# Optimization experiments

Hardware: AMD Instinct MI355X
Metric: run time of the kernel (lower is better)

## Reference

```python
import jax, jax.numpy as jnp
import numpy as np

# ---- static config ----
G = 4          # num graphs
NG = 512       # nodes per graph
N = G * NG     # total nodes
E = 32768      # num edges
IN_DIM = 128
HID = 32
HEADS = 4
HC = HID * HEADS  # 128
OUT_DIM = 32
N_LAYERS = 2
GRID = 500
Q = 20
NEG_SLOPE = 0.2
QUANTILES = jnp.asarray(np.linspace(0.0, 1.0, Q), jnp.float32)  # [Q]


def setup_inputs() -> dict:
    key = jax.random.key(0)
    ks = jax.random.split(key, 32)
    inp = {}
    inp['x'] = jax.random.normal(ks[0], (N, IN_DIM), jnp.float32)
    inp['edge_index'] = jax.random.randint(ks[1], (2, E), 0, N).astype(jnp.int64)
    inp['batch'] = (jnp.arange(N) // NG).astype(jnp.int64)
    # GATConv params (2 layers, both 128 -> 4 heads x 32, concat)
    for l, (kin,) in enumerate([(IN_DIM,), (HC,)]):
        s = 1.0 / np.sqrt(kin)
        inp[f'W{l}'] = jax.random.normal(ks[2 + 4 * l], (kin, HC), jnp.float32) * s
        inp[f'as{l}'] = jax.random.normal(ks[3 + 4 * l], (HEADS, HID), jnp.float32) * s
        inp[f'ad{l}'] = jax.random.normal(ks[4 + 4 * l], (HEADS, HID), jnp.float32) * s
        inp[f'b{l}'] = jnp.zeros((HC,), jnp.float32)
    for l in range(N_LAYERS + 1):
        inp[f'lpW{l}'] = jax.random.normal(ks[10 + 2 * l], (HC, OUT_DIM), jnp.float32) * (1.0 / np.sqrt(HC))
        inp[f'lpb{l}'] = jnp.zeros((OUT_DIM,), jnp.float32)
    for l in range(N_LAYERS + 1):
        inp[f'kW{l}'] = jax.random.normal(ks[16 + 2 * l], (HC * Q, OUT_DIM), jnp.float32) * (1.0 / np.sqrt(HC * Q))
        inp[f'kb{l}'] = jnp.zeros((OUT_DIM,), jnp.float32)
    inp['pool_w'] = jnp.ones((2,), jnp.float32) / 2.0
    inp['beta'] = jax.random.normal(ks[22], (OUT_DIM,), jnp.float32)
    inp['h0'] = jax.random.normal(ks[23], (1,), jnp.float32)
    return inp


def _gat_layer(x, src, dst, W, a_src, a_dst, bias):
    # PyG GATConv (concat=True, add_self_loops=True, negative_slope=0.2), eval mode
    n = x.shape[0]
    xh = (x @ W).reshape(n, HEADS, HID)              # [N,H,C]
    loop = jnp.arange(n)
    s = jnp.concatenate([src, loop])                 # [E+N]
    d = jnp.concatenate([dst, loop])
    al_s = jnp.einsum('nhc,hc->nh', xh, a_src)       # [N,H]
    al_d = jnp.einsum('nhc,hc->nh', xh, a_dst)
    e = jax.nn.leaky_relu(al_s[s] + al_d[d], NEG_SLOPE)   # [E+N,H]
    e_max = jax.ops.segment_max(e, d, num_segments=n)     # stable softmax per dst
    e = jnp.exp(e - e_max[d])
    denom = jax.ops.segment_sum(e, d, num_segments=n)
    alpha = e / (denom[d] + 1e-16)                   # [E+N,H]
    out = jax.ops.segment_sum(alpha[:, :, None] * xh[s], d, num_segments=n)
    return out.reshape(n, HC) + bias


def _kde_per_graph(xg):
    # xg: [Ng, D] -> [D*Q] soft-quantile features via grid KDE
    n = xg.shape[0]
    mn = xg.min(axis=0) - 1e-6                       # [D]
    mx = xg.max(axis=0) + 1e-6
    grid = jnp.linspace(0.0, 1.0, GRID)[:, None] * (mx - mn) + mn   # [Gp,D]
    std = xg.std(axis=0) + 1e-8 / 3
    h = 1.06 * std * float(n) ** (-0.2)              # [D]
    u = (grid[:, None, :] - xg[None, :, :]) / h      # [Gp,Ng,D]  (dominant tensor)
    kern = jnp.exp(-0.5 * u * u) / (h * np.sqrt(2.0 * np.pi))
    density = kern.mean(axis=1)                      # [Gp,D]
    cdf = jnp.cumsum(density, axis=0)
    cdf = cdf / jnp.clip(cdf[-1:], 1e-8)
    dist = jnp.abs(cdf[:, :, None] - QUANTILES)      # [Gp,D,Q]
    w = jax.nn.sigmoid(-100.0 * dist)
    w = w / (w.sum(axis=0, keepdims=True) + 1e-8)
    qv = (grid[:, :, None] * w).sum(axis=0)          # [D,Q]
    return qv.reshape(-1)


def _readout(cur, lpW, lpb, kW, kb, pool_w):
    xr = cur.reshape(G, NG, -1)
    pooled = jnp.stack([xr.mean(axis=1), xr.max(axis=1)], axis=0)   # [2,G,D]
    wp = (pooled * pool_w[:, None, None]).sum(axis=0)               # [G,D]
    h = wp @ lpW + lpb                                              # [G,out]
    kf = jax.vmap(_kde_per_graph)(xr)                               # [G,D*Q]
    return h, kf @ kW + kb


def reference(x, edge_index, batch, W0, as0, ad0, b0, W1, as1, ad1, b1,
              lpW0, lpb0, lpW1, lpb1, lpW2, lpb2,
              kW0, kb0, kW1, kb1, kW2, kb2, pool_w, beta, h0):
    src, dst = edge_index[0], edge_index[1]
    convs = [(W0, as0, ad0, b0), (W1, as1, ad1, b1)]
    lps = [(lpW0, lpb0), (lpW1, lpb1), (lpW2, lpb2)]
    kps = [(kW0, kb0), (kW1, kb1), (kW2, kb2)]
    cur = x
    h_list, kde_list = [], []
    for i in range(N_LAYERS):
        h, kp = _readout(cur, lps[i][0], lps[i][1], kps[i][0], kps[i][1], pool_w)
        h_list.append(h); kde_list.append(kp)
        cur = _gat_layer(cur, src, dst, *convs[i])
        if i != N_LAYERS - 1:
            cur = jax.nn.relu(cur)
    h, kp = _readout(cur, lps[-1][0], lps[-1][1], kps[-1][0], kps[-1][1], pool_w)
    h_list.append(h); kde_list.append(kp)
    main_out = jnp.stack(h_list).mean(axis=0)        # [G,out]
    kde_out = jnp.stack(kde_list).mean(axis=0)
    risk = (main_out + kde_out) @ beta + h0          # [G]
    return risk
```

## Files before the change

kernel.cpp:

```cpp
#include <hip/hip_runtime.h>
#include <math.h>

#define GNUM 4
#define NG 512
#define NN 2048
#define EE 32768
#define HC 128
#define HEADS 4
#define HID 32
#define GRID_PTS 500
#define QN 20
#define ODIM 32
#define MAXE 160

#define LOG2E 1.44269504088896340736f
#define NEG_HALF_LOG2E -0.72134752044448170368f
#define N_POW_M02 0.2871745887492588f
#define SIG_K 144.269504089f

__device__ __forceinline__ float fexp2(float x){ return __builtin_amdgcn_exp2f(x); }
__device__ __forceinline__ float frcp(float x){ return __builtin_amdgcn_rcpf(x); }

struct SmemKDE {
  __align__(16) float2 xs[NG];
  float4 wred4[8];
  float sc[4];
  float wsum[8], woff[9];
  float redw[QN][8], redg[QN][8];
  float qs[QN];
};
struct SmemXW  { float rows[4][HC]; };
struct SmemGat {
  int   ssrc[4][MAXE];
  float sexp[4][MAXE][HEADS];
  float smax[4][HEADS], sfac[4][HEADS];
};
union Smem { SmemKDE kde; SmemXW xw; SmemGat gat; };

__device__ void kde_phase(Smem& sm, const float* __restrict__ cur, int do_relu, int trans,
        const float* __restrict__ kW, const float* __restrict__ kb, float* __restrict__ kacc,
        const float* __restrict__ lpW, const float* __restrict__ lpb,
        const float* __restrict__ poolw, float* __restrict__ macc){
  int b = blockIdx.x;
  int g = b >> 7, d = b & 127;
  int t = threadIdx.x;
  int lane = t & 63, wave = t >> 6;
  float v = trans ? cur[(size_t)d*NN + g*NG + t]
                  : cur[((size_t)g*NG + t)*HC + d];
  if (do_relu) v = fmaxf(v, 0.f);
  sm.kde.xs[t] = make_float2(v, v*v);
  float mn=v, mx=v, smv=v, sq=v*v;
  #pragma unroll
  for (int m=32; m>0; m>>=1){
    mn = fminf(mn, __shfl_xor(mn, m, 64));
    mx = fmaxf(mx, __shfl_xor(mx, m, 64));
    smv += __shfl_xor(smv, m, 64);
    sq += __shfl_xor(sq, m, 64);
  }
  if (lane==0) sm.kde.wred4[wave] = make_float4(mn,mx,smv,sq);
  __syncthreads();
  if (t==0){
    float4 r = sm.kde.wred4[0];
    #pragma unroll
    for (int i=1;i<8;++i){
      float4 bb = sm.kde.wred4[i];
      r.x = fminf(r.x,bb.x); r.y = fmaxf(r.y,bb.y); r.z += bb.z; r.w += bb.w;
    }
    float mean = r.z * (1.f/NG);
    float var  = fmaxf(r.w*(1.f/NG) - mean*mean, 0.f);
    float sd   = sqrtf(var) + (1e-8f/3.f);
    float h    = 1.06f * sd * N_POW_M02;
    float lo = r.x - 1e-6f, hi = r.y + 1e-6f;
    sm.kde.sc[0] = lo;
    sm.kde.sc[1] = (hi-lo)*(1.f/(GRID_PTS-1));
    sm.kde.sc[2] = NEG_HALF_LOG2E/(h*h);
    sm.kde.sc[3] = poolw[0]*mean + poolw[1]*r.y;
  }
  __syncthreads();
  float lo = sm.kde.sc[0], st = sm.kde.sc[1], kk = sm.kde.sc[2];
  float gv = lo + st*(float)t;
  float acc = 0.f;
  if (t < GRID_PTS){
    float c0 = kk*gv*gv, c1 = -2.f*kk*gv;
    const float4* p4 = (const float4*)sm.kde.xs;
    #pragma unroll 4
    for (int i=0;i<NG/2;++i){
      float4 s2 = p4[i];
      acc += fexp2(fmaf(kk, s2.y, fmaf(c1, s2.x, c0)));
      acc += fexp2(fmaf(kk, s2.w, fmaf(c1, s2.z, c0)));
    }
  }
  float sv = acc;
  #pragma unroll
  for (int off=1; off<64; off<<=1){
    float n = __shfl_up(sv, off, 64);
    if (lane >= off) sv += n;
  }
  if (lane==63) sm.kde.wsum[wave] = sv;
  __syncthreads();
  if (t==0){
    float r2 = 0.f;
    #pragma unroll
    for (int i=0;i<8;++i){ sm.kde.woff[i]=r2; r2+=sm.kde.wsum[i]; }
    sm.kde.woff[8]=r2;
  }
  if (t < QN*8){ ((float*)sm.kde.redw)[t]=0.f; ((float*)sm.kde.redg)[t]=0.f; }
  __syncthreads();
  float invt = 1.f/fmaxf(sm.kde.woff[8], 1e-8f);
  float c = (sv + sm.kde.woff[wave]) * invt;
  float cw0 = __shfl(c, 0, 64), cw1 = __shfl(c, 63, 64);
  int qlo = max(0, (int)ceilf((cw0 - 0.17f)*(float)(QN-1)));
  int qhi = min(QN-1, (int)floorf((cw1 + 0.17f)*(float)(QN-1)));
  for (int q=qlo; q<=qhi; ++q){
    float w = 0.f;
    if (t < GRID_PTS){
      float dist = fabsf(c - (float)q*(1.f/(QN-1)));
      w = frcp(1.f + fexp2(SIG_K*dist));
    }
    float gw = gv*w;
    #pragma unroll
    for (int m=32;m>0;m>>=1){
      w  += __shfl_xor(w,  m, 64);
      gw += __shfl_xor(gw, m, 64);
    }
    if (lane==0){ sm.kde.redw[q][wave]=w; sm.kde.redg[q][wave]=gw; }
  }
  __syncthreads();
  if (t < QN){
    float sw=0.f, sgw=0.f;
    #pragma unroll
    for (int i=0;i<8;++i){ sw+=sm.kde.redw[t][i]; sgw+=sm.kde.redg[t][i]; }
    sm.kde.qs[t] = sgw / (sw + 1e-8f);
  }
  __syncthreads();
  if (t < ODIM){
    int shard = (d >> 5) & 3;
    float a = 0.f;
    const float* kwb = kW + (size_t)d*QN*ODIM + t;
    #pragma unroll
    for (int q=0;q<QN;++q) a += sm.kde.qs[q]*kwb[q*ODIM];
    if (d==0) a += kb[t];
    atomicAdd(&kacc[shard*128 + g*ODIM + t], a);
    float bb = sm.kde.sc[3]*lpW[d*ODIM + t];
    if (d==0) bb += lpb[t];
    atomicAdd(&macc[shard*128 + g*ODIM + t], bb);
  }
  __syncthreads();
}

__device__ float gather_core(Smem& sm, int d, int sub, int tl,
        const int* __restrict__ csr, const int* __restrict__ pos,
        const float* __restrict__ als, const float* __restrict__ ald,
        const float* __restrict__ xh, const float* __restrict__ bias){
  int deg = min(pos[d], MAXE-1);
  int E = deg + 1;
  const int* base = csr + d*MAXE;
  float a0 = ald[d*4+0], a1 = ald[d*4+1], a2 = ald[d*4+2], a3 = ald[d*4+3];
  for (int i=tl; i<E; i+=128){
    int s = (i < deg) ? base[i] : d;
    sm.gat.ssrc[sub][i] = s;
    float e0 = als[s*4+0]+a0, e1 = als[s*4+1]+a1, e2 = als[s*4+2]+a2, e3 = als[s*4+3]+a3;
    e0 = (e0>=0.f)? e0 : 0.2f*e0;
    e1 = (e1>=0.f)? e1 : 0.2f*e1;
    e2 = (e2>=0.f)? e2 : 0.2f*e2;
    e3 = (e3>=0.f)? e3 : 0.2f*e3;
    sm.gat.sexp[sub][i][0]=e0; sm.gat.sexp[sub][i][1]=e1;
    sm.gat.sexp[sub][i][2]=e2; sm.gat.sexp[sub][i][3]=e3;
  }
  __syncthreads();
  if (tl < HEADS){
    float m = -INFINITY;
    for (int i=0;i<E;++i) m = fmaxf(m, sm.gat.sexp[sub][i][tl]);
    sm.gat.smax[sub][tl] = m;
  }
  __syncthreads();
  for (int i=tl; i<E; i+=128){
    #pragma unroll
    for (int h=0;h<HEADS;++h)
      sm.gat.sexp[sub][i][h] = fexp2(LOG2E*(sm.gat.sexp[sub][i][h]-sm.gat.smax[sub][h]));
  }
  __syncthreads();
  if (tl < HEADS){
    float sdn = 0.f;
    for (int i=0;i<E;++i) sdn += sm.gat.sexp[sub][i][tl];
    sm.gat.sfac[sub][tl] = 1.f/(sdn + 1e-16f);
  }
  __syncthreads();
  int h = tl >> 5;
  float fac = sm.gat.sfac[sub][h];
  float acc = bias[tl];
  for (int i=0;i<E;++i)
    acc += sm.gat.sexp[sub][i][h]*fac * xh[(size_t)sm.gat.ssrc[sub][i]*HC + tl];
  __syncthreads();
  return acc;
}

__device__ void xw_emit(Smem& sm, int sub, int j, int n,
        const float* __restrict__ W, const float* __restrict__ as_, const float* __restrict__ ad_,
        float* __restrict__ xh, float* __restrict__ als, float* __restrict__ ald){
  float acc = 0.f;
  #pragma unroll 8
  for (int c2=0;c2<HC;++c2)
    acc += sm.xw.rows[sub][c2]*W[(size_t)c2*HC + j];
  xh[(size_t)n*HC + j] = acc;
  int h = j >> 5, cc = j & 31;
  float ps = acc*as_[h*HID+cc], pd = acc*ad_[h*HID+cc];
  #pragma unroll
  for (int m=16;m>0;m>>=1){
    ps += __shfl_xor(ps, m, 32);
    pd += __shfl_xor(pd, m, 32);
  }
  if (cc==0){ als[n*HEADS+h]=ps; ald[n*HEADS+h]=pd; }
}

__device__ void write_transposed(Smem& sm, int t, int n0, float* __restrict__ curT){
  if (t < HC){
    float4 v = make_float4(sm.xw.rows[0][t], sm.xw.rows[1][t],
                           sm.xw.rows[2][t], sm.xw.rows[3][t]);
    *(float4*)(curT + (size_t)t*NN + n0) = v;
  }
}

__global__ __launch_bounds__(1024) void k_zero(int* __restrict__ pos, float* __restrict__ acc){
  int t = threadIdx.x;
  pos[t] = 0; pos[t+1024] = 0;
  acc[t] = 0.f; acc[t+1024] = 0.f;
  if (t < 1024) acc[t+2048] = 0.f;
}

__global__ __launch_bounds__(512) void k_L0(const float* __restrict__ x,
        const float* __restrict__ kW, const float* __restrict__ kb, float* __restrict__ kacc,
        const float* __restrict__ lpW, const float* __restrict__ lpb,
        const float* __restrict__ poolw, float* __restrict__ macc,
        const float* __restrict__ W, const float* __restrict__ as_, const float* __restrict__ ad_,
        float* __restrict__ xh, float* __restrict__ als, float* __restrict__ ald,
        const int* __restrict__ src, const int* __restrict__ dst,
        int* __restrict__ pos, int* __restrict__ csr){
  __shared__ Smem sm;
  int t = threadIdx.x;
  if (blockIdx.x < 512){
    kde_phase(sm, x, 0, 0, kW, kb, kacc, lpW, lpb, poolw, macc);
  } else {
    int b2 = blockIdx.x - 512;
    if (t < 64){
      int e = b2*64 + t;
      int dd = dst[e];
      int pp = atomicAdd(&pos[dd], 1);
      if (pp < MAXE) csr[dd*MAXE + pp] = src[e];
    }
    int sub = t >> 7, j = t & 127;
    int n = b2*4 + sub;
    sm.xw.rows[sub][j] = x[(size_t)n*HC + j];
    __syncthreads();
    xw_emit(sm, sub, j, n, W, as_, ad_, xh, als, ald);
  }
}

__global__ __launch_bounds__(512) void k_G0(const int* __restrict__ csr, const int* __restrict__ pos,
        const float* __restrict__ als_in, const float* __restrict__ ald_in,
        const float* __restrict__ xh_in, const float* __restrict__ bias,
        float* __restrict__ cur1T,
        const float* __restrict__ W1, const float* __restrict__ as1, const float* __restrict__ ad1,
        float* __restrict__ xh2, float* __restrict__ als2, float* __restrict__ ald2){
  __shared__ Smem sm;
  int t = threadIdx.x;
  int sub = t >> 7, tl = t & 127;
  int d = blockIdx.x*4 + sub;
  float acc = gather_core(sm, d, sub, tl, csr, pos, als_in, ald_in, xh_in, bias);
  sm.xw.rows[sub][tl] = fmaxf(acc, 0.f);
  __syncthreads();
  write_transposed(sm, t, blockIdx.x*4, cur1T);
  xw_emit(sm, sub, tl, d, W1, as1, ad1, xh2, als2, ald2);
}

__global__ __launch_bounds__(512) void k_L1(const float* __restrict__ cur1T,
        const float* __restrict__ kW, const float* __restrict__ kb, float* __restrict__ kacc,
        const float* __restrict__ lpW, const float* __restrict__ lpb,
        const float* __restrict__ poolw, float* __restrict__ macc,
        const int* __restrict__ csr, const int* __restrict__ pos,
        const float* __restrict__ als2, const float* __restrict__ ald2,
        const float* __restrict__ xh2, const float* __restrict__ bias,
        float* __restrict__ cur2T){
  __shared__ Smem sm;
  int t = threadIdx.x;
  if (blockIdx.x < 512){
    kde_phase(sm, cur1T, 0, 1, kW, kb, kacc, lpW, lpb, poolw, macc);
  } else {
    int b2 = blockIdx.x - 512;
    int sub = t >> 7, tl = t & 127;
    int d = b2*4 + sub;
    float acc = gather_core(sm, d, sub, tl, csr, pos, als2, ald2, xh2, bias);
    sm.xw.rows[sub][tl] = acc;
    __syncthreads();
    write_transposed(sm, t, b2*4, cur2T);
  }
}

__global__ __launch_bounds__(512) void k_L2(const float* __restrict__ cur2T,
        const float* __restrict__ kW, const float* __restrict__ kb, float* __restrict__ kacc,
        const float* __restrict__ lpW, const float* __restrict__ lpb,
        const float* __restrict__ poolw, float* __restrict__ macc){
  __shared__ Smem sm;
  kde_phase(sm, cur2T, 0, 1, kW, kb, kacc, lpW, lpb, poolw, macc);
}

__global__ void k_final(const float* __restrict__ maccS, const float* __restrict__ kaccS,
                        const float* __restrict__ beta, const float* __restrict__ h0,
                        float* __restrict__ out){
  int t = threadIdx.x;
  int g = t >> 5, o = t & 31;
  __shared__ float sdm[128];
  float s3 = 0.f;
  #pragma unroll
  for (int l=0;l<3;++l)
    #pragma unroll
    for (int s=0;s<4;++s)
      s3 += maccS[l*512 + s*128 + t] + kaccS[l*512 + s*128 + t];
  sdm[t] = s3 * (1.f/3.f) * beta[o];
  __syncthreads();
  if ((t & 31) == 0){
    float s = 0.f;
    #pragma unroll
    for (int i=0;i<32;++i) s += sdm[g*32+i];
    out[g] = s + h0[0];
  }
}

extern "C" void kernel_launch(void* const* d_in, const int* in_sizes, int n_in,
                              void* d_out, int out_size, void* d_ws, size_t ws_size,
                              hipStream_t stream) {
  (void)in_sizes; (void)n_in; (void)out_size; (void)ws_size;
  const float* x    = (const float*)d_in[0];
  const int*   ei   = (const int*)d_in[1];
  const int*   srcp = ei;
  const int*   dstp = ei + EE;
  const float* W[2]   = {(const float*)d_in[3], (const float*)d_in[7]};
  const float* As[2]  = {(const float*)d_in[4], (const float*)d_in[8]};
  const float* Ad[2]  = {(const float*)d_in[5], (const float*)d_in[9]};
  const float* Bi[2]  = {(const float*)d_in[6], (const float*)d_in[10]};
  const float* lpW[3] = {(const float*)d_in[11], (const float*)d_in[13], (const float*)d_in[15]};
  const float* lpb[3] = {(const float*)d_in[12], (const float*)d_in[14], (const float*)d_in[16]};
  const float* kW[3]  = {(const float*)d_in[17], (const float*)d_in[19], (const float*)d_in[21]};
  const float* kb[3]  = {(const float*)d_in[18], (const float*)d_in[20], (const float*)d_in[22]};
  const float* poolw  = (const float*)d_in[23];
  const float* beta   = (const float*)d_in[24];
  const float* h0     = (const float*)d_in[25];
  float* out = (float*)d_out;

  float* ws = (float*)d_ws;
  float* cur1T = ws;
  float* cur2T = cur1T + 262144;
  float* xh    = cur2T + 262144;
  float* xh2   = xh + 262144;
  float* als   = xh2 + 262144;
  float* ald   = als + 8192;
  float* als2  = ald + 8192;
  float* ald2  = als2 + 8192;
  float* maccS = ald2 + 8192;
  float* kaccS = maccS + 1536;
  int*   pos   = (int*)(kaccS + 1536);
  int*   csr   = pos + 2048;

  k_zero<<<1, 1024, 0, stream>>>(pos, maccS);
  k_L0<<<1024, 512, 0, stream>>>(x, kW[0], kb[0], kaccS, lpW[0], lpb[0], poolw, maccS,
                                 W[0], As[0], Ad[0], xh, als, ald,
                                 srcp, dstp, pos, csr);
  k_G0<<<512, 512, 0, stream>>>(csr, pos, als, ald, xh, Bi[0], cur1T,
                                W[1], As[1], Ad[1], xh2, als2, ald2);
  k_L1<<<1024, 512, 0, stream>>>(cur1T, kW[1], kb[1], kaccS+512, lpW[1], lpb[1], poolw, maccS+512,
                                 csr, pos, als2, ald2, xh2, Bi[1], cur2T);
  k_L2<<<512, 512, 0, stream>>>(cur2T, kW[2], kb[2], kaccS+1024, lpW[2], lpb[2], poolw, maccS+1024);
  k_final<<<1, 128, 0, stream>>>(maccS, kaccS, beta, h0, out);
}
```

Before: 201.1 us.

## Bucket KDE samples and evaluate only those within kernel radius per wave

```diff
diff --git a/kernel.cpp b/kernel.cpp
--- a/kernel.cpp
+++ b/kernel.cpp
@@ -12,6 +12,7 @@
 #define QN 20
 #define ODIM 32
 #define MAXE 160
+#define NBUK 16
 
 #define LOG2E 1.44269504088896340736f
 #define NEG_HALF_LOG2E -0.72134752044448170368f
@@ -24,10 +25,11 @@
 struct SmemKDE {
   __align__(16) float2 xs[NG];
   float4 wred4[8];
-  float sc[4];
+  float sc[8];
   float wsum[8], woff[9];
   float redw[QN][8], redg[QN][8];
   float qs[QN];
+  int bcnt[NBUK], bstart[NBUK+1], bcur[NBUK];
 };
 struct SmemXW  { float rows[4][HC]; };
 struct SmemGat {
@@ -48,7 +50,6 @@
   float v = trans ? cur[(size_t)d*NN + g*NG + t]
                   : cur[((size_t)g*NG + t)*HC + d];
   if (do_relu) v = fmaxf(v, 0.f);
-  sm.kde.xs[t] = make_float2(v, v*v);
   float mn=v, mx=v, smv=v, sq=v*v;
   #pragma unroll
   for (int m=32; m>0; m>>=1){
@@ -58,6 +59,7 @@
     sq += __shfl_xor(sq, m, 64);
   }
   if (lane==0) sm.kde.wred4[wave] = make_float4(mn,mx,smv,sq);
+  if (t < NBUK) sm.kde.bcnt[t] = 0;
   __syncthreads();
   if (t==0){
     float4 r = sm.kde.wred4[0];
@@ -75,19 +77,41 @@
     sm.kde.sc[1] = (hi-lo)*(1.f/(GRID_PTS-1));
     sm.kde.sc[2] = NEG_HALF_LOG2E/(h*h);
     sm.kde.sc[3] = poolw[0]*mean + poolw[1]*r.y;
+    sm.kde.sc[4] = (float)NBUK/(hi-lo);
+    sm.kde.sc[5] = 5.f*h;
   }
   __syncthreads();
   float lo = sm.kde.sc[0], st = sm.kde.sc[1], kk = sm.kde.sc[2];
+  float bscale = sm.kde.sc[4], R = sm.kde.sc[5];
+  int bkt = min(NBUK-1, max(0, (int)((v - lo)*bscale)));
+  atomicAdd(&sm.kde.bcnt[bkt], 1);
+  __syncthreads();
+  if (t==0){
+    int run=0;
+    #pragma unroll
+    for (int i=0;i<NBUK;++i){ int c=sm.kde.bcnt[i]; sm.kde.bstart[i]=run; run+=c; }
+    sm.kde.bstart[NBUK]=run;
+  }
+  __syncthreads();
+  if (t < NBUK) sm.kde.bcur[t] = sm.kde.bstart[t];
+  __syncthreads();
+  int p = atomicAdd(&sm.kde.bcur[bkt], 1);
+  sm.kde.xs[p] = make_float2(v, v*v);
+  __syncthreads();
   float gv = lo + st*(float)t;
   float acc = 0.f;
-  if (t < GRID_PTS){
-    float c0 = kk*gv*gv, c1 = -2.f*kk*gv;
-    const float4* p4 = (const float4*)sm.kde.xs;
-    #pragma unroll 4
-    for (int i=0;i<NG/2;++i){
-      float4 s2 = p4[i];
-      acc += fexp2(fmaf(kk, s2.y, fmaf(c1, s2.x, c0)));
-      acc += fexp2(fmaf(kk, s2.w, fmaf(c1, s2.z, c0)));
+  {
+    float gvw0 = lo + st*(float)(wave<<6);
+    float gvw1 = lo + st*(float)((wave<<6)+63);
+    int blo = max(0, (int)((gvw0 - R - lo)*bscale));
+    int bhi = min(NBUK-1, (int)((gvw1 + R - lo)*bscale));
+    int i0 = sm.kde.bstart[blo], i1 = sm.kde.bstart[bhi+1];
+    if (t < GRID_PTS){
+      float c0 = kk*gv*gv, c1 = -2.f*kk*gv;
+      for (int i=i0; i<i1; ++i){
+        float2 s = sm.kde.xs[i];
+        acc += fexp2(fmaf(kk, s.y, fmaf(c1, s.x, c0)));
+      }
     }
   }
   float sv = acc;
```

Result: slower. 228.4 us (+13.6%).
